# Kernel tuning notes

Measured on AMD Instinct MI355X. Metric: run time of the kernel, lower is better.

## Reference

```python
import jax, jax.numpy as jnp
import numpy as np

KSIZE = 15
SIGMA = 3.0
PAD = KSIZE // 2


def _gauss_kernel2d():
    g = jnp.arange(KSIZE, dtype=jnp.float32) - KSIZE // 2
    g = jnp.exp(-(g ** 2) / (2.0 * SIGMA * SIGMA))
    g = g / g.sum()
    return g[:, None] * g[None, :]  # [15,15]


def _depthwise_blur(x, k2):
    # x: [B,C,H,W]; 15x15 Gaussian applied per channel (matches per-channel F.conv2d loop)
    C = x.shape[1]
    kernel = jnp.broadcast_to(k2[None, None], (C, 1, KSIZE, KSIZE))
    return jax.lax.conv_general_dilated(
        x, kernel, window_strides=(1, 1), padding=[(PAD, PAD), (PAD, PAD)],
        feature_group_count=C, dimension_numbers=("NCHW", "OIHW", "NCHW"))


def setup_inputs() -> dict:
    key = jax.random.key(0)
    B, C, H, W = 4, 3, 1024, 1024
    x = jax.random.uniform(key, (B, C, H, W), dtype=jnp.float32)
    f32 = lambda v: jnp.asarray(v, dtype=jnp.float32)
    return {
        "x": x,
        "gains": jnp.array([1.1, 1.0, 0.9], dtype=jnp.float32),
        "gamma": f32(0.9),
        "shadow_boost": f32(0.1),
        "highlight_reduce": f32(0.1),
        "brightness": f32(0.05),
        "contrast": f32(1.1),
        "enhance_amount": f32(0.8),
        "softness": f32(0.6),
        "intensity": f32(0.3),
        "rotation": f32(30.0),
        "hardness": f32(2.0),
    }


def reference(x, gains, gamma, shadow_boost, highlight_reduce, brightness,
              contrast, enhance_amount, softness, intensity, rotation, hardness):
    B, C, H, W = x.shape
    k2 = _gauss_kernel2d()

    # WhiteBalanceAdjustment
    x = x * gains.reshape(1, C, 1, 1)
    # ToneCurveAdjustment
    x = jnp.power(x, gamma)
    # ShadowHighlightEnhancement
    hi = jax.nn.sigmoid((x - 0.5) * 10.0)
    x = jnp.clip(x + shadow_boost * (1.0 - hi) - highlight_reduce * hi, 0.0, 1.0)
    # GlobalBrightnessContrastAdjustment
    x = jnp.clip(contrast * (x - 0.5) + 0.5 + brightness, 0.0, 1.0)
    # LocalContrastEnhancement
    local_mean = _depthwise_blur(x, k2)
    x = x + enhance_amount * (x - local_mean)
    # SoftnessFilter
    blurred = _depthwise_blur(x, k2)
    x = softness * blurred + (1.0 - softness) * x
    # GradientNDAdjustment
    ys = jnp.linspace(-1.0, 1.0, H, dtype=jnp.float32)
    xs = jnp.linspace(-1.0, 1.0, W, dtype=jnp.float32)
    grid_y, grid_x = jnp.meshgrid(ys, xs, indexing="ij")
    theta = rotation * (np.pi / 180.0)
    grid_rot = grid_x * jnp.cos(theta) + grid_y * jnp.sin(theta)
    mask = jax.nn.sigmoid(-hardness * grid_rot)[None, None]  # [1,1,H,W]
    x = jnp.clip(x * (1.0 - intensity * mask), 0.0, 1.0)

    return jnp.clip(x, 0.0, 1.0)
```

## Files before the change

kernel.cpp:

```cpp
#include <hip/hip_runtime.h>
#include <math.h>

#define HH 1024
#define WW 1024
#define NPLANES 12
#define PLANE (HH * WW)
#define NTOT (NPLANES * PLANE)

#define TW 64
#define TH 64
#define HR 78
#define PITCH 68

struct W15 { float w[15]; };

__device__ inline float4 ld4z(const float* __restrict__ row, int x) {
    if (x >= 0 && x + 3 < WW) return *(const float4*)(row + x);
    float4 r; float* p = (float*)&r;
#pragma unroll
    for (int j = 0; j < 4; ++j) { int xx = x + j; p[j] = (xx >= 0 && xx < WW) ? row[xx] : 0.0f; }
    return r;
}

__device__ inline float chain1(float t, float gain, float gamma, float sb,
                               float hr, float br, float ct) {
    t = t * gain;
    t = __builtin_amdgcn_exp2f(gamma * __log2f(t));
    float hi = __fdividef(1.0f, 1.0f + __expf((0.5f - t) * 10.0f));
    t = t + sb * (1.0f - hi) - hr * hi;
    t = fminf(fmaxf(t, 0.0f), 1.0f);
    t = ct * (t - 0.5f) + 0.5f + br;
    return fminf(fmaxf(t, 0.0f), 1.0f);
}

__device__ inline float4 hdot4(const float* f, const W15& wk) {
    float4 o; float* po = (float*)&o;
#pragma unroll
    for (int j = 0; j < 4; ++j) {
        float a = 0.0f, b = 0.0f;
#pragma unroll
        for (int k = 0; k < 8; ++k)  a += wk.w[k] * f[j + 1 + k];
#pragma unroll
        for (int k = 8; k < 15; ++k) b += wk.w[k] * f[j + 1 + k];
        po[j] = a + b;
    }
    return o;
}

__global__ __launch_bounds__(256) void k_point(
    const float4* __restrict__ x, float4* __restrict__ o,
    const float* __restrict__ gains,
    const float* __restrict__ pg, const float* __restrict__ psb,
    const float* __restrict__ phr, const float* __restrict__ pbr,
    const float* __restrict__ pct)
{
    int i = blockIdx.x * blockDim.x + threadIdx.x;
    if (i >= NTOT / 4) return;
    int c = ((i * 4) / PLANE) % 3;
    float gain = gains[c];
    float gamma = *pg, sb = *psb, hr = *phr, br = *pbr, ct = *pct;

    float4 v = x[i];
    float* pv = (float*)&v;
#pragma unroll
    for (int j = 0; j < 4; ++j)
        pv[j] = chain1(pv[j], gain, gamma, sb, hr, br, ct);
    o[i] = v;
}

__device__ inline void tile_map(int& p, int& x0, int& y0, bool& edge) {
    int L = (blockIdx.z * gridDim.y + blockIdx.y) * gridDim.x + blockIdx.x;
    int xcd = L & 7;
    int t   = L >> 3;
    int g   = xcd * 384 + t;
    p = g >> 8;
    int w  = g & 255;
    int ty = w >> 4, tx = w & 15;
    x0 = tx * TW; y0 = ty * TH;
    edge = (tx == 0) || (tx == 15) || (ty == 0) || (ty == 15);
}

__device__ inline void ldrow20(float* f, const float* rp) {
    *(float4*)&f[0]  = *(const float4*)(rp);
    *(float4*)&f[4]  = *(const float4*)(rp + 4);
    *(float4*)&f[8]  = *(const float4*)(rp + 8);
    *(float4*)&f[12] = *(const float4*)(rp + 12);
    *(float4*)&f[16] = *(const float4*)(rp + 16);
}

__device__ inline void hblur_stage(const float* __restrict__ plane, float* __restrict__ hbl,
                                   int x0, int y0, int tid, bool edge, const W15& wk)
{
    const int cx = (tid & 15) * 4;
    const int r0 = tid >> 4;
    if (!edge) {
        const float* base = plane + (size_t)(y0 - 7) * WW + (x0 + cx - 8);
        float f[2][20];
        ldrow20(f[0], base + (size_t)r0 * WW);
#pragma unroll
        for (int it = 0; it < 5; ++it) {
            int r  = r0 + 16 * it;
            int rn = r + 16;
            if (it < 4 && rn < HR)
                ldrow20(f[(it + 1) & 1], base + (size_t)rn * WW);
            if (r < HR)
                *(float4*)&hbl[r * PITCH + cx] = hdot4(f[it & 1], wk);
        }
    } else {
        for (int it = 0; it < 5; ++it) {
            int r = r0 + 16 * it;
            if (r < HR) {
                int gy = y0 - 7 + r;
                float4 o;
                if (gy >= 0 && gy < HH) {
                    const float* row = plane + (size_t)gy * WW;
                    int xb = x0 + cx - 8;
                    float f[20];
                    *(float4*)&f[0]  = ld4z(row, xb);
                    *(float4*)&f[4]  = ld4z(row, xb + 4);
                    *(float4*)&f[8]  = ld4z(row, xb + 8);
                    *(float4*)&f[12] = ld4z(row, xb + 12);
                    *(float4*)&f[16] = ld4z(row, xb + 16);
                    o = hdot4(f, wk);
                } else {
                    o = make_float4(0.0f, 0.0f, 0.0f, 0.0f);
                }
                *(float4*)&hbl[r * PITCH + cx] = o;
            }
        }
    }
}

__global__ __launch_bounds__(256) void k_blur_lce(
    const float* __restrict__ t0, float* __restrict__ x2,
    const float* __restrict__ penh, W15 wk)
{
    __shared__ float hbl[HR * PITCH];
    int p, x0, y0; bool edge;
    tile_map(p, x0, y0, edge);
    const int tid = threadIdx.x;
    const float* plane = t0 + (size_t)p * PLANE;

    hblur_stage(plane, hbl, x0, y0, tid, edge, wk);
    __syncthreads();

    const int tx  = tid & 63;
    const int ty  = tid >> 6;
    const int ly0 = ty * 16;
    const int gx  = x0 + tx;
    const float e = *penh;

    float cc[16];
#pragma unroll
    for (int j = 0; j < 16; ++j) cc[j] = plane[(size_t)(y0 + ly0 + j) * WW + gx];

    float win[15];
#pragma unroll
    for (int k = 0; k < 15; ++k) win[k] = hbl[(ly0 + k) * PITCH + tx];

    float* dstP = x2 + (size_t)p * PLANE;
#pragma unroll
    for (int j = 0; j < 16; ++j) {
        int y = y0 + ly0 + j;
        float a = 0.0f, b = 0.0f;
#pragma unroll
        for (int k = 0; k < 8; ++k)  a += wk.w[k] * win[k];
#pragma unroll
        for (int k = 8; k < 15; ++k) b += wk.w[k] * win[k];
        float lm = a + b;
        dstP[(size_t)y * WW + gx] = (1.0f + e) * cc[j] - e * lm;
#pragma unroll
        for (int k = 0; k < 14; ++k) win[k] = win[k + 1];
        win[14] = hbl[(ly0 + j + 15) * PITCH + tx];
    }
}

__global__ __launch_bounds__(256) void k_blur_final(
    const float* __restrict__ x2, float* __restrict__ dst,
    const float* __restrict__ psoft, const float* __restrict__ pint,
    const float* __restrict__ prot, const float* __restrict__ phard, W15 wk)
{
    __shared__ float hbl[HR * PITCH];
    int p, x0, y0; bool edge;
    tile_map(p, x0, y0, edge);
    const int tid = threadIdx.x;
    const float* plane = x2 + (size_t)p * PLANE;

    hblur_stage(plane, hbl, x0, y0, tid, edge, wk);
    __syncthreads();

    const int tx  = tid & 63;
    const int ty  = tid >> 6;
    const int ly0 = ty * 16;
    const int gx  = x0 + tx;

    const float s     = *psoft;
    const float inten = *pint;
    const float hard  = *phard;
    const float theta = (*prot) * 0.017453292519943295f;
    const float cth = __cosf(theta), sth = __sinf(theta);
    const float base = (-1.0f + 2.0f * (float)gx * (1.0f / (float)(WW - 1))) * cth;

    float cc[16];
#pragma unroll
    for (int j = 0; j < 16; ++j) cc[j] = plane[(size_t)(y0 + ly0 + j) * WW + gx];

    float win[15];
#pragma unroll
    for (int k = 0; k < 15; ++k) win[k] = hbl[(ly0 + k) * PITCH + tx];

    float* dstP = dst + (size_t)p * PLANE;
#pragma unroll
    for (int j = 0; j < 16; ++j) {
        int y = y0 + ly0 + j;
        float a = 0.0f, b = 0.0f;
#pragma unroll
        for (int k = 0; k < 8; ++k)  a += wk.w[k] * win[k];
#pragma unroll
        for (int k = 8; k < 15; ++k) b += wk.w[k] * win[k];
        float bl = a + b;
        float v = s * bl + (1.0f - s) * cc[j];
        float gyf = -1.0f + 2.0f * (float)y * (1.0f / (float)(HH - 1));
        float mask = __fdividef(1.0f, 1.0f + __expf(hard * (base + gyf * sth)));
        v = v * (1.0f - inten * mask);
        v = fminf(fmaxf(v, 0.0f), 1.0f);
        dstP[(size_t)y * WW + gx] = v;
#pragma unroll
        for (int k = 0; k < 14; ++k) win[k] = win[k + 1];
        win[14] = hbl[(ly0 + j + 15) * PITCH + tx];
    }
}

extern "C" void kernel_launch(void* const* d_in, const int* in_sizes, int n_in,
                              void* d_out, int out_size, void* d_ws, size_t ws_size,
                              hipStream_t stream)
{
    const float* x       = (const float*)d_in[0];
    const float* gains   = (const float*)d_in[1];
    const float* p_gamma = (const float*)d_in[2];
    const float* p_sb    = (const float*)d_in[3];
    const float* p_hr    = (const float*)d_in[4];
    const float* p_br    = (const float*)d_in[5];
    const float* p_ct    = (const float*)d_in[6];
    const float* p_enh   = (const float*)d_in[7];
    const float* p_soft  = (const float*)d_in[8];
    const float* p_int   = (const float*)d_in[9];
    const float* p_rot   = (const float*)d_in[10];
    const float* p_hard  = (const float*)d_in[11];

    float* T0  = (float*)d_out;
    float* X2  = (float*)d_ws;
    float* OUT = (float*)d_out;

    W15 wk;
    {
        double g[15], sum = 0.0;
        for (int i = 0; i < 15; ++i) { double d = (double)(i - 7); g[i] = exp(-d * d / 18.0); sum += g[i]; }
        for (int i = 0; i < 15; ++i) wk.w[i] = (float)(g[i] / sum);
    }

    k_point<<<dim3(NTOT / 4 / 256), dim3(256), 0, stream>>>(
        (const float4*)x, (float4*)T0, gains, p_gamma, p_sb, p_hr, p_br, p_ct);

    dim3 grid(WW / TW, HH / TH, NPLANES);
    k_blur_lce<<<grid, dim3(256), 0, stream>>>(T0, X2, p_enh, wk);
    k_blur_final<<<grid, dim3(256), 0, stream>>>(X2, OUT, p_soft, p_int, p_rot, p_hard, wk);
}
```

Baseline: 187.4 us.

## Fuse pointwise chain and both blurs into one tiled kernel

Replaces three kernels (pointwise tone chain, local-contrast blur, softness blur) with a single kernel. Each 64x64 tile loads a 92x96 halo of the raw input, applies the tone chain, and stores it in XOR-swizzled shared memory. Both separable blurs are then computed in shared memory, using linearity to get the second blur as the blur of x2. This removes the intermediate global writes and reads of T0 and X2 and two launches. In exchange the halo is larger, so the pointwise chain is recomputed on overlap and more shared memory is used, which may lower occupancy.

```diff
diff --git a/kernel.cpp b/kernel.cpp
--- a/kernel.cpp
+++ b/kernel.cpp
@@ -5,22 +5,16 @@
 #define WW 1024
 #define NPLANES 12
 #define PLANE (HH * WW)
-#define NTOT (NPLANES * PLANE)
 
 #define TW 64
 #define TH 64
-#define HR 78
-#define PITCH 68
+#define RROWS 92
+#define PA 96
+#define PB 80
+#define P1 80
+#define PC 64
 
 struct W15 { float w[15]; };
-
-__device__ inline float4 ld4z(const float* __restrict__ row, int x) {
-    if (x >= 0 && x + 3 < WW) return *(const float4*)(row + x);
-    float4 r; float* p = (float*)&r;
-#pragma unroll
-    for (int j = 0; j < 4; ++j) { int xx = x + j; p[j] = (xx >= 0 && xx < WW) ? row[xx] : 0.0f; }
-    return r;
-}
 
 __device__ inline float chain1(float t, float gain, float gamma, float sb,
                                float hr, float br, float ct) {
@@ -47,25 +41,13 @@
     return o;
 }
 
-__global__ __launch_bounds__(256) void k_point(
-    const float4* __restrict__ x, float4* __restrict__ o,
-    const float* __restrict__ gains,
-    const float* __restrict__ pg, const float* __restrict__ psb,
-    const float* __restrict__ phr, const float* __restrict__ pbr,
-    const float* __restrict__ pct)
-{
-    int i = blockIdx.x * blockDim.x + threadIdx.x;
-    if (i >= NTOT / 4) return;
-    int c = ((i * 4) / PLANE) % 3;
-    float gain = gains[c];
-    float gamma = *pg, sb = *psb, hr = *phr, br = *pbr, ct = *pct;
-
-    float4 v = x[i];
-    float* pv = (float*)&v;
-#pragma unroll
-    for (int j = 0; j < 4; ++j)
-        pv[j] = chain1(pv[j], gain, gamma, sb, hr, br, ct);
-    o[i] = v;
+__device__ inline float dot15(const float* win, const W15& wk) {
+    float a = 0.0f, b = 0.0f;
+#pragma unroll
+    for (int k = 0; k < 8; ++k)  a += wk.w[k] * win[k];
+#pragma unroll
+    for (int k = 8; k < 15; ++k) b += wk.w[k] * win[k];
+    return a + b;
 }
 
 __device__ inline void tile_map(int& p, int& x0, int& y0, bool& edge) {
@@ -80,154 +62,171 @@
     edge = (tx == 0) || (tx == 15) || (ty == 0) || (ty == 15);
 }
 
-__device__ inline void ldrow20(float* f, const float* rp) {
-    *(float4*)&f[0]  = *(const float4*)(rp);
-    *(float4*)&f[4]  = *(const float4*)(rp + 4);
-    *(float4*)&f[8]  = *(const float4*)(rp + 8);
-    *(float4*)&f[12] = *(const float4*)(rp + 12);
-    *(float4*)&f[16] = *(const float4*)(rp + 16);
-}
-
-__device__ inline void hblur_stage(const float* __restrict__ plane, float* __restrict__ hbl,
-                                   int x0, int y0, int tid, bool edge, const W15& wk)
+__global__ __launch_bounds__(256) void k_fused(
+    const float* __restrict__ x, float* __restrict__ dst,
+    const float* __restrict__ gains,
+    const float* __restrict__ pg, const float* __restrict__ psb,
+    const float* __restrict__ phr, const float* __restrict__ pbr,
+    const float* __restrict__ pct, const float* __restrict__ penh,
+    const float* __restrict__ psoft, const float* __restrict__ pint,
+    const float* __restrict__ prot, const float* __restrict__ phard,
+    W15 wk)
 {
-    const int cx = (tid & 15) * 4;
-    const int r0 = tid >> 4;
-    if (!edge) {
-        const float* base = plane + (size_t)(y0 - 7) * WW + (x0 + cx - 8);
-        float f[2][20];
-        ldrow20(f[0], base + (size_t)r0 * WW);
-#pragma unroll
-        for (int it = 0; it < 5; ++it) {
-            int r  = r0 + 16 * it;
-            int rn = r + 16;
-            if (it < 4 && rn < HR)
-                ldrow20(f[(it + 1) & 1], base + (size_t)rn * WW);
-            if (r < HR)
-                *(float4*)&hbl[r * PITCH + cx] = hdot4(f[it & 1], wk);
-        }
-    } else {
-        for (int it = 0; it < 5; ++it) {
-            int r = r0 + 16 * it;
-            if (r < HR) {
-                int gy = y0 - 7 + r;
-                float4 o;
-                if (gy >= 0 && gy < HH) {
-                    const float* row = plane + (size_t)gy * WW;
-                    int xb = x0 + cx - 8;
-                    float f[20];
-                    *(float4*)&f[0]  = ld4z(row, xb);
-                    *(float4*)&f[4]  = ld4z(row, xb + 4);
-                    *(float4*)&f[8]  = ld4z(row, xb + 8);
-                    *(float4*)&f[12] = ld4z(row, xb + 12);
-                    *(float4*)&f[16] = ld4z(row, xb + 16);
-                    o = hdot4(f, wk);
-                } else {
-                    o = make_float4(0.0f, 0.0f, 0.0f, 0.0f);
-                }
-                *(float4*)&hbl[r * PITCH + cx] = o;
-            }
-        }
-    }
-}
-
-__global__ __launch_bounds__(256) void k_blur_lce(
-    const float* __restrict__ t0, float* __restrict__ x2,
-    const float* __restrict__ penh, W15 wk)
-{
-    __shared__ float hbl[HR * PITCH];
+    __shared__ float A [RROWS * PA];
+    __shared__ float Bb[RROWS * PB];
+
     int p, x0, y0; bool edge;
     tile_map(p, x0, y0, edge);
     const int tid = threadIdx.x;
-    const float* plane = t0 + (size_t)p * PLANE;
-
-    hblur_stage(plane, hbl, x0, y0, tid, edge, wk);
-    __syncthreads();
-
     const int tx  = tid & 63;
     const int ty  = tid >> 6;
-    const int ly0 = ty * 16;
-    const int gx  = x0 + tx;
-    const float e = *penh;
+
+    const float* __restrict__ plane = x + (size_t)p * PLANE;
+    const float gain  = gains[p % 3];
+    const float gamma = *pg, sb = *psb, hr = *phr, br = *pbr, ct = *pct;
+
+    if (!edge) {
+        const float* base = plane + (size_t)(y0 - 14) * WW + (x0 - 16);
+        auto do1 = [&](int c) {
+            int r = c / 24, c4 = c % 24;
+            float4 v = *(const float4*)(base + (size_t)r * WW + 4 * c4);
+            float* pv = (float*)&v;
+#pragma unroll
+            for (int q = 0; q < 4; ++q)
+                pv[q] = chain1(pv[q], gain, gamma, sb, hr, br, ct);
+            *(float4*)&A[r * PA + ((c4 ^ (r & 7)) << 2)] = v;
+        };
+#pragma unroll
+        for (int it = 0; it < 8; ++it) do1(tid + 256 * it);
+        if (tid < 160) do1(tid + 2048);
+    } else {
+        auto do1e = [&](int c) {
+            int r = c / 24, c4 = c % 24;
+            int gy  = y0 - 14 + r;
+            int gx0 = x0 - 16 + 4 * c4;
+            float4 v = make_float4(0.f, 0.f, 0.f, 0.f);
+            if ((unsigned)gy < HH) {
+                const float* row = plane + (size_t)gy * WW;
+                float* pv = (float*)&v;
+                if (gx0 >= 0 && gx0 + 3 < WW) {
+                    v = *(const float4*)(row + gx0);
+#pragma unroll
+                    for (int q = 0; q < 4; ++q)
+                        pv[q] = chain1(pv[q], gain, gamma, sb, hr, br, ct);
+                } else {
+#pragma unroll
+                    for (int q = 0; q < 4; ++q) {
+                        int gx = gx0 + q;
+                        if ((unsigned)gx < WW)
+                            pv[q] = chain1(row[gx], gain, gamma, sb, hr, br, ct);
+                    }
+                }
+            }
+            *(float4*)&A[r * PA + ((c4 ^ (r & 7)) << 2)] = v;
+        };
+#pragma unroll
+        for (int it = 0; it < 8; ++it) do1e(tid + 256 * it);
+        if (tid < 160) do1e(tid + 2048);
+    }
+    __syncthreads();
 
     float cc[16];
 #pragma unroll
-    for (int j = 0; j < 16; ++j) cc[j] = plane[(size_t)(y0 + ly0 + j) * WW + gx];
-
-    float win[15];
-#pragma unroll
-    for (int k = 0; k < 15; ++k) win[k] = hbl[(ly0 + k) * PITCH + tx];
-
-    float* dstP = x2 + (size_t)p * PLANE;
-#pragma unroll
     for (int j = 0; j < 16; ++j) {
-        int y = y0 + ly0 + j;
-        float a = 0.0f, b = 0.0f;
-#pragma unroll
-        for (int k = 0; k < 8; ++k)  a += wk.w[k] * win[k];
-#pragma unroll
-        for (int k = 8; k < 15; ++k) b += wk.w[k] * win[k];
-        float lm = a + b;
-        dstP[(size_t)y * WW + gx] = (1.0f + e) * cc[j] - e * lm;
-#pragma unroll
-        for (int k = 0; k < 14; ++k) win[k] = win[k + 1];
-        win[14] = hbl[(ly0 + j + 15) * PITCH + tx];
-    }
-}
-
-__global__ __launch_bounds__(256) void k_blur_final(
-    const float* __restrict__ x2, float* __restrict__ dst,
-    const float* __restrict__ psoft, const float* __restrict__ pint,
-    const float* __restrict__ prot, const float* __restrict__ phard, W15 wk)
-{
-    __shared__ float hbl[HR * PITCH];
-    int p, x0, y0; bool edge;
-    tile_map(p, x0, y0, edge);
-    const int tid = threadIdx.x;
-    const float* plane = x2 + (size_t)p * PLANE;
-
-    hblur_stage(plane, hbl, x0, y0, tid, edge, wk);
-    __syncthreads();
-
-    const int tx  = tid & 63;
-    const int ty  = tid >> 6;
-    const int ly0 = ty * 16;
-    const int gx  = x0 + tx;
-
+        int rr = ty * 16 + j + 14;
+        cc[j] = A[rr * PA + ((((tx >> 2) + 4) ^ (rr & 7)) << 2) + (tx & 3)];
+    }
+    {
+        auto do2 = [&](int c) {
+            int r = c / 20, j4 = c % 20;
+            int rx = r & 7;
+            float f[20];
+#pragma unroll
+            for (int i = 0; i < 5; ++i)
+                *(float4*)&f[4 * i] =
+                    *(const float4*)&A[r * PA + (((j4 + i) ^ rx) << 2)];
+            *(float4*)&Bb[r * PB + 4 * j4] = hdot4(f, wk);
+        };
+#pragma unroll
+        for (int it = 0; it < 7; ++it) do2(tid + 256 * it);
+        if (tid < 48) do2(tid + 1792);
+    }
+    __syncthreads();
+
+    float* B1 = A;
+    if (tid < 240) {
+        int j    = tid % 80;
+        int band = tid / 80;
+        int r1s  = band * 26;
+        bool xin = (unsigned)(x0 - 8 + j) < WW;
+        float win[15];
+#pragma unroll
+        for (int k = 0; k < 14; ++k) win[k] = Bb[(r1s + k) * PB + j];
+#pragma unroll
+        for (int jj = 0; jj < 26; ++jj) {
+            win[14] = Bb[(r1s + jj + 14) * PB + j];
+            float v = dot15(win, wk);
+            if (edge) {
+                int gy = y0 - 7 + r1s + jj;
+                if (!((unsigned)gy < HH) || !xin) v = 0.0f;
+            }
+            B1[(r1s + jj) * P1 + j] = v;
+#pragma unroll
+            for (int k = 0; k < 14; ++k) win[k] = win[k + 1];
+        }
+    }
+    __syncthreads();
+
+    float bb[16];
+#pragma unroll
+    for (int j = 0; j < 16; ++j)
+        bb[j] = B1[(ty * 16 + j + 7) * P1 + (tx + 8)];
+    float* C = Bb;
+    {
+        auto do4 = [&](int c) {
+            int r = c >> 4, j4 = c & 15;
+            float f[20];
+#pragma unroll
+            for (int i = 0; i < 5; ++i)
+                *(float4*)&f[4 * i] = *(const float4*)&B1[r * P1 + 4 * (j4 + i)];
+            *(float4*)&C[r * PC + 4 * j4] = hdot4(f, wk);
+        };
+#pragma unroll
+        for (int it = 0; it < 4; ++it) do4(tid + 256 * it);
+        if (tid < 224) do4(tid + 1024);
+    }
+    __syncthreads();
+
+    const float e     = *penh;
     const float s     = *psoft;
     const float inten = *pint;
     const float hard  = *phard;
     const float theta = (*prot) * 0.017453292519943295f;
     const float cth = __cosf(theta), sth = __sinf(theta);
-    const float base = (-1.0f + 2.0f * (float)gx * (1.0f / (float)(WW - 1))) * cth;
-
-    float cc[16];
-#pragma unroll
-    for (int j = 0; j < 16; ++j) cc[j] = plane[(size_t)(y0 + ly0 + j) * WW + gx];
+    const int   gx    = x0 + tx;
+    const float gbase = (-1.0f + 2.0f * (float)gx * (1.0f / (float)(WW - 1))) * cth;
+    const float ce    = 1.0f + e;
 
     float win[15];
 #pragma unroll
-    for (int k = 0; k < 15; ++k) win[k] = hbl[(ly0 + k) * PITCH + tx];
-
-    float* dstP = dst + (size_t)p * PLANE;
-#pragma unroll
-    for (int j = 0; j < 16; ++j) {
-        int y = y0 + ly0 + j;
-        float a = 0.0f, b = 0.0f;
-#pragma unroll
-        for (int k = 0; k < 8; ++k)  a += wk.w[k] * win[k];
-#pragma unroll
-        for (int k = 8; k < 15; ++k) b += wk.w[k] * win[k];
-        float bl = a + b;
-        float v = s * bl + (1.0f - s) * cc[j];
-        float gyf = -1.0f + 2.0f * (float)y * (1.0f / (float)(HH - 1));
-        float mask = __fdividef(1.0f, 1.0f + __expf(hard * (base + gyf * sth)));
+    for (int k = 0; k < 14; ++k) win[k] = C[(ty * 16 + k) * PC + tx];
+
+    float* __restrict__ dstP = dst + (size_t)p * PLANE;
+#pragma unroll
+    for (int jj = 0; jj < 16; ++jj) {
+        win[14] = C[(ty * 16 + jj + 14) * PC + tx];
+        float B2  = dot15(win, wk);
+        float x2c = ce * cc[jj] - e * bb[jj];
+        float bx2 = ce * bb[jj] - e * B2;
+        float v   = s * bx2 + (1.0f - s) * x2c;
+        int   y   = y0 + ty * 16 + jj;
+        float gyn = -1.0f + 2.0f * (float)y * (1.0f / (float)(HH - 1));
+        float mask = __fdividef(1.0f, 1.0f + __expf(hard * (gbase + gyn * sth)));
         v = v * (1.0f - inten * mask);
         v = fminf(fmaxf(v, 0.0f), 1.0f);
         dstP[(size_t)y * WW + gx] = v;
 #pragma unroll
         for (int k = 0; k < 14; ++k) win[k] = win[k + 1];
-        win[14] = hbl[(ly0 + j + 15) * PITCH + tx];
     }
 }
 
@@ -248,10 +247,6 @@
     const float* p_rot   = (const float*)d_in[10];
     const float* p_hard  = (const float*)d_in[11];
 
-    float* T0  = (float*)d_out;
-    float* X2  = (float*)d_ws;
-    float* OUT = (float*)d_out;
-
     W15 wk;
     {
         double g[15], sum = 0.0;
@@ -259,10 +254,8 @@
         for (int i = 0; i < 15; ++i) wk.w[i] = (float)(g[i] / sum);
     }
 
-    k_point<<<dim3(NTOT / 4 / 256), dim3(256), 0, stream>>>(
-        (const float4*)x, (float4*)T0, gains, p_gamma, p_sb, p_hr, p_br, p_ct);
-
     dim3 grid(WW / TW, HH / TH, NPLANES);
-    k_blur_lce<<<grid, dim3(256), 0, stream>>>(T0, X2, p_enh, wk);
-    k_blur_final<<<grid, dim3(256), 0, stream>>>(X2, OUT, p_soft, p_int, p_rot, p_hard, wk);
-}
+    k_fused<<<grid, dim3(256), 0, stream>>>(
+        x, (float*)d_out, gains, p_gamma, p_sb, p_hr, p_br, p_ct,
+        p_enh, p_soft, p_int, p_rot, p_hard, wk);
+}
```

Result: slower. 202.6 us (+8.1%).
